# Kernel tuning notes

Hardware: AMD Instinct MI355X
Metric: run time of the kernel (lower is better)

The kernel has to match this reference:

```python
import jax, jax.numpy as jnp
import numpy as np

B, CHI, CHO, H, W = 2, 256, 256, 128, 128
K = 9  # 3x3 kernel taps


def setup_inputs() -> dict:
    key = jax.random.key(0)
    ks = jax.random.split(key, 9)
    x = jax.random.normal(ks[0], (B, CHI, H, W), jnp.float32)
    centerness = jax.random.uniform(ks[1], (B, 1, H, W), jnp.float32)
    scale = jax.random.normal(ks[2], (B, 1, H, W), jnp.float32)
    # 1x1 conv weights stored as [out_ch, in_ch] (kernel dims squeezed)
    offset_w = jax.random.normal(ks[3], (2 * K, 1), jnp.float32) * 0.5
    offset_b = jax.random.normal(ks[4], (2 * K,), jnp.float32) * 0.5
    mask_w = jax.random.normal(ks[5], (K, 1), jnp.float32)
    mask_b = jax.random.normal(ks[6], (K,), jnp.float32) * 0.1
    fan_in = CHI * K
    conv_w = jax.random.normal(ks[7], (CHO, CHI, 3, 3), jnp.float32) / np.sqrt(fan_in).astype(np.float32)
    conv_b = jax.random.normal(ks[8], (CHO,), jnp.float32) * 0.01
    return {"x": x, "centerness": centerness, "scale": scale,
            "offset_w": offset_w, "offset_b": offset_b,
            "mask_w": mask_w, "mask_b": mask_b,
            "conv_w": conv_w, "conv_b": conv_b}


def _bilinear_sample(img, ys, xs):
    # img: [C, Hi, Wi]; ys, xs: [K, H, W] float sampling coords.
    # Out-of-bounds corners contribute zero (DCNv2 zero-padding semantics).
    C, Hi, Wi = img.shape
    y0 = jnp.floor(ys)
    x0 = jnp.floor(xs)
    wy1 = ys - y0
    wx1 = xs - x0
    wy0 = 1.0 - wy1
    wx0 = 1.0 - wx1
    imgf = img.reshape(C, Hi * Wi)

    def corner(yc, xc):
        valid = (yc >= 0) & (yc <= Hi - 1) & (xc >= 0) & (xc <= Wi - 1)
        yi = jnp.clip(yc, 0, Hi - 1).astype(jnp.int32)
        xi = jnp.clip(xc, 0, Wi - 1).astype(jnp.int32)
        v = jnp.take(imgf, yi * Wi + xi, axis=1)  # [C, K, H, W]
        return v * valid.astype(img.dtype)[None]

    out = (corner(y0, x0) * (wy0 * wx0)[None]
           + corner(y0, x0 + 1.0) * (wy0 * wx1)[None]
           + corner(y0 + 1.0, x0) * (wy1 * wx0)[None]
           + corner(y0 + 1.0, x0 + 1.0) * (wy1 * wx1)[None])
    return out  # [C, K, H, W]


def reference(x, centerness, scale, offset_w, offset_b, mask_w, mask_b, conv_w, conv_b):
    Bn, C, Hn, Wn = x.shape
    cho = conv_w.shape[0]
    # 1x1 convs producing offsets [B, 2K, H, W] and sigmoid mask [B, K, H, W]
    off = jnp.einsum('bihw,oi->bohw', scale, offset_w) + offset_b[None, :, None, None]
    msk = jax.nn.sigmoid(jnp.einsum('bihw,oi->bohw', centerness, mask_w)
                         + mask_b[None, :, None, None])
    dy = off[:, 0::2]  # [B, K, H, W]
    dx = off[:, 1::2]
    # base 3x3 tap displacements (pad=1, dilation=1, stride=1)
    kidx = jnp.arange(K)
    ky = (kidx // 3 - 1).astype(x.dtype)
    kx = (kidx % 3 - 1).astype(x.dtype)
    yy = jnp.arange(Hn, dtype=x.dtype)
    xx = jnp.arange(Wn, dtype=x.dtype)
    ys = yy[None, None, :, None] + ky[None, :, None, None] + dy  # [B, K, H, W]
    xs = xx[None, None, None, :] + kx[None, :, None, None] + dx
    sampled = jax.vmap(_bilinear_sample)(x, ys, xs)  # [B, C, K, H, W]
    sampled = sampled * msk[:, None]  # modulated by mask
    out = jnp.einsum('bckhw,ock->bohw', sampled, conv_w.reshape(cho, C, K))
    return out + conv_b[None, :, None, None]
```

## Files before the change

### kernel.cpp

```cpp
#include <hip/hip_runtime.h>


typedef __bf16 bf16x8 __attribute__((ext_vector_type(8)));
typedef float f32x4 __attribute__((ext_vector_type(4)));

#define HH 128
#define WW 128
#define CIN 256
#define COUT 256
#define KK9 9
#define HW (HH * WW)
#define KDIM (KK9 * CIN)
#define XT_PER_B (HW * CIN)

__device__ __forceinline__ ushort f2bf(float f) {
  union { float f; unsigned u; } v; v.f = f;
  unsigned u = v.u;
  u += 0x7FFFu + ((u >> 16) & 1u);
  return (ushort)(u >> 16);
}
__device__ __forceinline__ float bf2f(ushort h) {
  return __uint_as_float(((unsigned)h) << 16);
}
__device__ __forceinline__ float bfsel(const int4 v, int e) {
  int w = ((e >> 1) == 0) ? v.x : ((e >> 1) == 1) ? v.y
        : ((e >> 1) == 2) ? v.z : v.w;
  return __uint_as_float((e & 1) ? ((unsigned)w & 0xffff0000u)
                                 : ((unsigned)w << 16));
}
__device__ __forceinline__ int packpair(const float4 wt, const int4 a0,
                                        const int4 a1, const int4 a2,
                                        const int4 a3, int q) {
  float vl = wt.x * bfsel(a0, 2 * q)     + wt.y * bfsel(a1, 2 * q)
           + wt.z * bfsel(a2, 2 * q)     + wt.w * bfsel(a3, 2 * q);
  float vh = wt.x * bfsel(a0, 2 * q + 1) + wt.y * bfsel(a1, 2 * q + 1)
           + wt.z * bfsel(a2, 2 * q + 1) + wt.w * bfsel(a3, 2 * q + 1);
  return (int)((unsigned)f2bf(vl) | ((unsigned)f2bf(vh) << 16));
}

__global__ __launch_bounds__(256) void k_transpose(const float* __restrict__ x,
                                                   ushort* __restrict__ xT) {
  __shared__ ushort tile[64][130];
  const int bid = blockIdx.x;
  const int y  = bid & 127;
  const int t  = bid >> 7;
  const int cb = t & 3;
  const int b  = t >> 2;
  const int xl = threadIdx.x & 127;
  const int ch = threadIdx.x >> 7;
  const float* src = x + (size_t)(b * CIN + cb * 64) * HW + y * WW + xl;
#pragma unroll
  for (int i = 0; i < 32; ++i) {
    int c = ch * 32 + i;
    tile[c][xl] = f2bf(src[(size_t)c * HW]);
  }
  __syncthreads();
  const int c  = threadIdx.x & 63;
  const int xh = threadIdx.x >> 6;
  ushort* dst = xT + (size_t)b * XT_PER_B + (size_t)(y * WW) * CIN + cb * 64 + c;
#pragma unroll
  for (int i = 0; i < 32; ++i) {
    int xx = xh * 32 + i;
    dst[(size_t)xx * CIN] = tile[c][xx];
  }
}

__global__ __launch_bounds__(256) void k_packw2(const float* __restrict__ cw,
                                                ushort* __restrict__ Bm2) {
  int idx = blockIdx.x * 256 + threadIdx.x;
  int e  = idx & 7;
  int l  = (idx >> 3) & 63;
  int f  = idx >> 9;
  int ni = f & 15;
  int s  = f >> 4;
  int cc = s & 7;
  int t  = s >> 3;
  int nl = l & 15;
  int kg = l >> 4;
  int o  = ni * 16 + nl;
  int c  = cc * 32 + kg * 8 + e;
  Bm2[idx] = f2bf(cw[(o * CIN + c) * KK9 + t]);
}

__global__ __launch_bounds__(64) void k_mfma9(
    const ushort* __restrict__ xT, const ushort* __restrict__ Bm2,
    const float* __restrict__ scale, const float* __restrict__ ctr,
    const float* __restrict__ offw, const float* __restrict__ offb,
    const float* __restrict__ mskw, const float* __restrict__ mskb,
    const float* __restrict__ convb, float* __restrict__ out) {
  __shared__ int4   moff[32 * KK9];
  __shared__ float4 mwt[32 * KK9];

  const int lane = threadIdx.x;
  const int mb  = ((blockIdx.x & 7) << 7) | (blockIdx.x >> 3);
  const int b   = mb >> 9;
  const int rem = mb & 511;
  const int h   = rem >> 2;
  const int w0  = (rem & 3) << 5;

  for (int idx = lane; idx < 32 * KK9; idx += 64) {
    int p = idx / 9;
    int k = idx - p * 9;
    int w = w0 + p;
    float sc = scale[b * HW + h * WW + w];
    float ct = ctr[b * HW + h * WW + w];
    float dy = sc * offw[2 * k]     + offb[2 * k];
    float dx = sc * offw[2 * k + 1] + offb[2 * k + 1];
    float mk = 1.0f / (1.0f + __expf(-(ct * mskw[k] + mskb[k])));
    float ys = (float)(h + (k / 3) - 1) + dy;
    float xs = (float)(w + (k % 3) - 1) + dx;
    float y0 = floorf(ys), x0 = floorf(xs);
    float wy1 = ys - y0, wx1 = xs - x0;
    float wy0 = 1.f - wy1, wx0 = 1.f - wx1;
    int offc[4]; float wtc[4];
#pragma unroll
    for (int a = 0; a < 2; ++a)
#pragma unroll
      for (int bb = 0; bb < 2; ++bb) {
        float yc = y0 + (float)a, xc = x0 + (float)bb;
        bool valid = (yc >= 0.f) && (yc <= 127.f) && (xc >= 0.f) && (xc <= 127.f);
        int yi = (int)fminf(fmaxf(yc, 0.f), 127.f);
        int xi = (int)fminf(fmaxf(xc, 0.f), 127.f);
        offc[a * 2 + bb] = (yi * WW + xi) * CIN;
        wtc[a * 2 + bb]  = (a ? wy1 : wy0) * (bb ? wx1 : wx0) * mk * (valid ? 1.f : 0.f);
      }
    moff[idx] = make_int4(offc[0], offc[1], offc[2], offc[3]);
    mwt[idx]  = make_float4(wtc[0], wtc[1], wtc[2], wtc[3]);
  }
  __syncthreads();

  const ushort* xTb = xT + (size_t)b * XT_PER_B;
  const int nl  = lane & 15;
  const int kg  = lane >> 4;
  const int kg8 = kg * 8;

  f32x4 acc0[16], acc1[16];
#pragma unroll
  for (int ni = 0; ni < 16; ++ni) {
    acc0[ni] = (f32x4){0.f, 0.f, 0.f, 0.f};
    acc1[ni] = (f32x4){0.f, 0.f, 0.f, 0.f};
  }

  const ushort* bpl = Bm2 + (size_t)lane * 8;

  for (int t = 0; t < KK9; ++t) {
    const int4   mo0 = moff[nl * 9 + t];
    const float4 wt0 = mwt[nl * 9 + t];
    const int4   mo1 = moff[(16 + nl) * 9 + t];
    const float4 wt1 = mwt[(16 + nl) * 9 + t];
    const ushort* s00 = xTb + mo0.x;
    const ushort* s01 = xTb + mo0.y;
    const ushort* s02 = xTb + mo0.z;
    const ushort* s03 = xTb + mo0.w;
    const ushort* s10 = xTb + mo1.x;
    const ushort* s11 = xTb + mo1.y;
    const ushort* s12 = xTb + mo1.z;
    const ushort* s13 = xTb + mo1.w;
#pragma unroll
    for (int cc = 0; cc < 8; ++cc) {
      const int ca = cc * 32 + kg8;
      int4 A00 = *(const int4*)(s00 + ca);
      int4 A01 = *(const int4*)(s01 + ca);
      int4 A02 = *(const int4*)(s02 + ca);
      int4 A03 = *(const int4*)(s03 + ca);
      int4 A10 = *(const int4*)(s10 + ca);
      int4 A11 = *(const int4*)(s11 + ca);
      int4 A12 = *(const int4*)(s12 + ca);
      int4 A13 = *(const int4*)(s13 + ca);
      int4 F0, F1;
      F0.x = packpair(wt0, A00, A01, A02, A03, 0);
      F0.y = packpair(wt0, A00, A01, A02, A03, 1);
      F0.z = packpair(wt0, A00, A01, A02, A03, 2);
      F0.w = packpair(wt0, A00, A01, A02, A03, 3);
      F1.x = packpair(wt1, A10, A11, A12, A13, 0);
      F1.y = packpair(wt1, A10, A11, A12, A13, 1);
      F1.z = packpair(wt1, A10, A11, A12, A13, 2);
      F1.w = packpair(wt1, A10, A11, A12, A13, 3);
      bf16x8 af0 = *reinterpret_cast<const bf16x8*>(&F0);
      bf16x8 af1 = *reinterpret_cast<const bf16x8*>(&F1);
      const ushort* bs = bpl + (size_t)(t * 8 + cc) * 8192;
#pragma unroll
      for (int ni = 0; ni < 16; ++ni) {
        int4 Bv = *(const int4*)(bs + ni * 512);
        bf16x8 bfr = *reinterpret_cast<const bf16x8*>(&Bv);
        acc0[ni] = __builtin_amdgcn_mfma_f32_16x16x32_bf16(af0, bfr, acc0[ni], 0, 0, 0);
        acc1[ni] = __builtin_amdgcn_mfma_f32_16x16x32_bf16(af1, bfr, acc1[ni], 0, 0, 0);
      }
    }
  }

#pragma unroll
  for (int ni = 0; ni < 16; ++ni) {
    int o = ni * 16 + nl;
    float cbv = convb[o];
    float* op = out + (size_t)(b * COUT + o) * HW + h * WW + w0;
#pragma unroll
    for (int r = 0; r < 4; ++r) {
      op[kg * 4 + r]      = acc0[ni][r] + cbv;
      op[16 + kg * 4 + r] = acc1[ni][r] + cbv;
    }
  }
}

extern "C" void kernel_launch(void* const* d_in, const int* in_sizes, int n_in,
                              void* d_out, int out_size, void* d_ws, size_t ws_size,
                              hipStream_t stream) {
  const float* x     = (const float*)d_in[0];
  const float* ctr   = (const float*)d_in[1];
  const float* scale = (const float*)d_in[2];
  const float* offw  = (const float*)d_in[3];
  const float* offb  = (const float*)d_in[4];
  const float* mskw  = (const float*)d_in[5];
  const float* mskb  = (const float*)d_in[6];
  const float* cw    = (const float*)d_in[7];
  const float* cb    = (const float*)d_in[8];
  float* out = (float*)d_out;

  char* ws = (char*)d_ws;
  ushort* xT  = (ushort*)ws;
  ushort* Bm2 = (ushort*)(ws + 16777216);

  k_transpose<<<dim3(1024), dim3(256), 0, stream>>>(x, xT);
  k_packw2<<<dim3(2304), dim3(256), 0, stream>>>(cw, Bm2);
  k_mfma9<<<dim3(1024), dim3(64), 0, stream>>>(xT, Bm2, scale, ctr, offw, offb,
                                               mskw, mskb, cb, out);
}
```

Measured before the change: 157.4 us.

## Split channel reduction across two blocks with atomic accumulation into bias-initialized output

Splits the input-channel reduction of the deformable conv GEMM in half, so each output tile is computed by two wavefronts (2048 blocks instead of 1024), each covering four of the eight channel chunks. A new kernel first fills the output with the conv bias, and the GEMM blocks add their partial sums using float atomicAdd. The aim is more parallelism and occupancy on a GPU where 1024 single-wave blocks underfill the CUs. The cost is an extra full-output write pass, atomic traffic on 32M floats, duplicated offset/mask setup per block, and a nondeterministic summation order.

```diff
diff --git a/kernel.cpp b/kernel.cpp
--- a/kernel.cpp
+++ b/kernel.cpp
@@ -82,21 +82,30 @@
   Bm2[idx] = f2bf(cw[(o * CIN + c) * KK9 + t]);
 }
 
-__global__ __launch_bounds__(64) void k_mfma9(
+__global__ __launch_bounds__(256) void k_init(const float* __restrict__ convb,
+                                              float* __restrict__ out) {
+  int i = blockIdx.x * 256 + threadIdx.x;
+  int o = (i >> 14) & 255;
+  out[i] = convb[o];
+}
+
+__global__ __launch_bounds__(64) void k_mfma11(
     const ushort* __restrict__ xT, const ushort* __restrict__ Bm2,
     const float* __restrict__ scale, const float* __restrict__ ctr,
     const float* __restrict__ offw, const float* __restrict__ offb,
     const float* __restrict__ mskw, const float* __restrict__ mskb,
-    const float* __restrict__ convb, float* __restrict__ out) {
+    float* __restrict__ out) {
   __shared__ int4   moff[32 * KK9];
   __shared__ float4 mwt[32 * KK9];
 
   const int lane = threadIdx.x;
-  const int mb  = ((blockIdx.x & 7) << 7) | (blockIdx.x >> 3);
-  const int b   = mb >> 9;
-  const int rem = mb & 511;
-  const int h   = rem >> 2;
-  const int w0  = (rem & 3) << 5;
+  const int mb_lin = ((blockIdx.x & 7) << 8) | (blockIdx.x >> 3);
+  const int tile = mb_lin >> 1;
+  const int kh   = mb_lin & 1;
+  const int b    = tile >> 9;
+  const int rem  = tile & 511;
+  const int h    = rem >> 2;
+  const int w0   = (rem & 3) << 5;
 
   for (int idx = lane; idx < 32 * KK9; idx += 64) {
     int p = idx / 9;
@@ -133,6 +142,7 @@
   const int nl  = lane & 15;
   const int kg  = lane >> 4;
   const int kg8 = kg * 8;
+  const int cc0 = kh * 4;
 
   f32x4 acc0[16], acc1[16];
 #pragma unroll
@@ -157,7 +167,8 @@
     const ushort* s12 = xTb + mo1.z;
     const ushort* s13 = xTb + mo1.w;
 #pragma unroll
-    for (int cc = 0; cc < 8; ++cc) {
+    for (int ccl = 0; ccl < 4; ++ccl) {
+      const int cc = cc0 + ccl;
       const int ca = cc * 32 + kg8;
       int4 A00 = *(const int4*)(s00 + ca);
       int4 A01 = *(const int4*)(s01 + ca);
@@ -192,12 +203,11 @@
 #pragma unroll
   for (int ni = 0; ni < 16; ++ni) {
     int o = ni * 16 + nl;
-    float cbv = convb[o];
     float* op = out + (size_t)(b * COUT + o) * HW + h * WW + w0;
 #pragma unroll
     for (int r = 0; r < 4; ++r) {
-      op[kg * 4 + r]      = acc0[ni][r] + cbv;
-      op[16 + kg * 4 + r] = acc1[ni][r] + cbv;
+      atomicAdd(&op[kg * 4 + r],      acc0[ni][r]);
+      atomicAdd(&op[16 + kg * 4 + r], acc1[ni][r]);
     }
   }
 }
@@ -222,6 +232,7 @@
 
   k_transpose<<<dim3(1024), dim3(256), 0, stream>>>(x, xT);
   k_packw2<<<dim3(2304), dim3(256), 0, stream>>>(cw, Bm2);
-  k_mfma9<<<dim3(1024), dim3(64), 0, stream>>>(xT, Bm2, scale, ctr, offw, offb,
-                                               mskw, mskb, cb, out);
-}
+  k_init<<<dim3(32768), dim3(256), 0, stream>>>(cb, out);
+  k_mfma11<<<dim3(2048), dim3(64), 0, stream>>>(xT, Bm2, scale, ctr, offw, offb,
+                                                mskw, mskb, out);
+}
```

Measured after the change: 336.9 us. 114% more time.

## Split channel reduction across two waves per block with LDS partial-sum combine

Applied to the files above, without the earlier changes.

The main MFMA kernel now runs two wavefronts per block, and each one handles half of the input-channel chunks for every tap. Wave 1 writes its accumulators to shared memory, and wave 0 adds them in along with the bias before storing. This doubles the number of waves working on each output tile, which adds latency hiding and parallelism for a grid of only 1024 single-wave blocks. The costs are 32 KB of extra LDS per block, a synchronisation barrier, and a serial reduction epilogue.

```diff
diff --git a/kernel.cpp b/kernel.cpp
--- a/kernel.cpp
+++ b/kernel.cpp
@@ -82,7 +82,7 @@
   Bm2[idx] = f2bf(cw[(o * CIN + c) * KK9 + t]);
 }
 
-__global__ __launch_bounds__(64) void k_mfma9(
+__global__ __launch_bounds__(128, 2) void k_mfma12(
     const ushort* __restrict__ xT, const ushort* __restrict__ Bm2,
     const float* __restrict__ scale, const float* __restrict__ ctr,
     const float* __restrict__ offw, const float* __restrict__ offb,
@@ -90,15 +90,18 @@
     const float* __restrict__ convb, float* __restrict__ out) {
   __shared__ int4   moff[32 * KK9];
   __shared__ float4 mwt[32 * KK9];
-
-  const int lane = threadIdx.x;
+  __shared__ f32x4  part[32][64];
+
+  const int tid  = threadIdx.x;
+  const int lane = tid & 63;
+  const int wid  = tid >> 6;
   const int mb  = ((blockIdx.x & 7) << 7) | (blockIdx.x >> 3);
   const int b   = mb >> 9;
   const int rem = mb & 511;
   const int h   = rem >> 2;
   const int w0  = (rem & 3) << 5;
 
-  for (int idx = lane; idx < 32 * KK9; idx += 64) {
+  for (int idx = tid; idx < 32 * KK9; idx += 128) {
     int p = idx / 9;
     int k = idx - p * 9;
     int w = w0 + p;
@@ -133,6 +136,7 @@
   const int nl  = lane & 15;
   const int kg  = lane >> 4;
   const int kg8 = kg * 8;
+  const int cc0 = wid * 4;
 
   f32x4 acc0[16], acc1[16];
 #pragma unroll
@@ -157,7 +161,8 @@
     const ushort* s12 = xTb + mo1.z;
     const ushort* s13 = xTb + mo1.w;
 #pragma unroll
-    for (int cc = 0; cc < 8; ++cc) {
+    for (int ccl = 0; ccl < 4; ++ccl) {
+      const int cc = cc0 + ccl;
       const int ca = cc * 32 + kg8;
       int4 A00 = *(const int4*)(s00 + ca);
       int4 A01 = *(const int4*)(s01 + ca);
@@ -189,15 +194,28 @@
     }
   }
 
-#pragma unroll
-  for (int ni = 0; ni < 16; ++ni) {
-    int o = ni * 16 + nl;
-    float cbv = convb[o];
-    float* op = out + (size_t)(b * COUT + o) * HW + h * WW + w0;
-#pragma unroll
-    for (int r = 0; r < 4; ++r) {
-      op[kg * 4 + r]      = acc0[ni][r] + cbv;
-      op[16 + kg * 4 + r] = acc1[ni][r] + cbv;
+  if (wid == 1) {
+#pragma unroll
+    for (int ni = 0; ni < 16; ++ni) {
+      part[ni][lane]      = acc0[ni];
+      part[16 + ni][lane] = acc1[ni];
+    }
+  }
+  __syncthreads();
+
+  if (wid == 0) {
+#pragma unroll
+    for (int ni = 0; ni < 16; ++ni) {
+      int o = ni * 16 + nl;
+      float cbv = convb[o];
+      f32x4 p0 = part[ni][lane];
+      f32x4 p1 = part[16 + ni][lane];
+      float* op = out + (size_t)(b * COUT + o) * HW + h * WW + w0;
+#pragma unroll
+      for (int r = 0; r < 4; ++r) {
+        op[kg * 4 + r]      = acc0[ni][r] + p0[r] + cbv;
+        op[16 + kg * 4 + r] = acc1[ni][r] + p1[r] + cbv;
+      }
     }
   }
 }
@@ -222,6 +240,6 @@
 
   k_transpose<<<dim3(1024), dim3(256), 0, stream>>>(x, xT);
   k_packw2<<<dim3(2304), dim3(256), 0, stream>>>(cw, Bm2);
-  k_mfma9<<<dim3(1024), dim3(64), 0, stream>>>(xT, Bm2, scale, ctr, offw, offb,
-                                               mskw, mskb, cb, out);
-}
+  k_mfma12<<<dim3(1024), dim3(128), 0, stream>>>(xT, Bm2, scale, ctr, offw, offb,
+                                                 mskw, mskb, cb, out);
+}
```

After: 266.9 us. +69.5%, slower.
